# Kernel tuning notes

Hardware: AMD Instinct MI355X
Metric: run time of the kernel (lower is better)

The kernel has to match this reference:

```python
import jax, jax.numpy as jnp
import numpy as np

B, S, H, L, NH, DH, V, FF, WD, W = 16, 512, 768, 12, 12, 64, 30522, 3072, 256, 255
T = S - 1


def layer_norm(x, s, b, eps=1e-12):
    m = jnp.mean(x, -1, keepdims=True)
    v = jnp.mean((x - m) ** 2, -1, keepdims=True)
    return (x - m) * jax.lax.rsqrt(v + eps) * s + b


def setup_inputs() -> dict:
    key = jax.random.key(0)
    ks = jax.random.split(key, 20)
    rng = np.random.RandomState(0)
    # ragged structure: words per sentence and wordpieces per word
    sent_lens = rng.randint(128, W + 1, size=B)
    token_lens = np.zeros((B, W), dtype=np.int32)
    for i in range(B):
        token_lens[i, : sent_lens[i]] = rng.randint(1, 3, size=sent_lens[i])
    bert_len = token_lens.sum(1)  # wordpieces per sentence (no CLS/SEP)
    attention_mask = (np.arange(S)[None, :] < (bert_len + 2)[:, None]).astype(np.int32)
    input_ids = rng.randint(0, V, size=(B, S)).astype(np.int32)
    sd = 0.02
    rn = lambda k, sh: jax.random.normal(k, sh, jnp.float32) * sd
    inp = {
        "input_ids": jnp.asarray(input_ids),
        "attention_mask": jnp.asarray(attention_mask),
        "token_lens": jnp.asarray(token_lens),
        "word_emb": rn(ks[0], (V, H)),
        "pos_emb": rn(ks[1], (S, H)),
        "type_emb": rn(ks[2], (2, H)),
        "emb_ln_s": jnp.ones((H,), jnp.float32),
        "emb_ln_b": jnp.zeros((H,), jnp.float32),
        "Wq": rn(ks[3], (L, H, H)), "bq": jnp.zeros((L, H), jnp.float32),
        "Wk": rn(ks[4], (L, H, H)), "bk": jnp.zeros((L, H), jnp.float32),
        "Wv": rn(ks[5], (L, H, H)), "bv": jnp.zeros((L, H), jnp.float32),
        "Wo": rn(ks[6], (L, H, H)), "bo": jnp.zeros((L, H), jnp.float32),
        "ln1_s": jnp.ones((L, H), jnp.float32), "ln1_b": jnp.zeros((L, H), jnp.float32),
        "W1": rn(ks[7], (L, H, FF)), "b1": jnp.zeros((L, FF), jnp.float32),
        "W2": rn(ks[8], (L, FF, H)), "b2": jnp.zeros((L, H), jnp.float32),
        "ln2_s": jnp.ones((L, H), jnp.float32), "ln2_b": jnp.zeros((L, H), jnp.float32),
        "proj_W": rn(ks[9], (H, WD)), "proj_b": jnp.zeros((WD,), jnp.float32),
    }
    return inp


def reference(input_ids, attention_mask, token_lens, word_emb, pos_emb, type_emb,
              emb_ln_s, emb_ln_b, Wq, bq, Wk, bk, Wv, bv, Wo, bo, ln1_s, ln1_b,
              W1, b1, W2, b2, ln2_s, ln2_b, proj_W, proj_b):
    # --- BERT embeddings ---
    h = word_emb[input_ids] + pos_emb[None, :, :] + type_emb[0][None, None, :]
    h = layer_norm(h, emb_ln_s, emb_ln_b)
    att_bias = (1.0 - attention_mask.astype(jnp.float32))[:, None, None, :] * -10000.0

    def block(h, p):
        wq, bq_, wk, bk_, wv, bv_, wo, bo_, l1s, l1b, w1, b1_, w2, b2_, l2s, l2b = p
        q = (h @ wq + bq_).reshape(B, S, NH, DH)
        k = (h @ wk + bk_).reshape(B, S, NH, DH)
        v = (h @ wv + bv_).reshape(B, S, NH, DH)
        scores = jnp.einsum('bqnd,bknd->bnqk', q, k) / np.float32(np.sqrt(DH)) + att_bias
        a = jax.nn.softmax(scores, axis=-1)
        ctx = jnp.einsum('bnqk,bknd->bqnd', a, v).reshape(B, S, H)
        h = layer_norm(h + ctx @ wo + bo_, l1s, l1b)
        f = jax.nn.gelu(h @ w1 + b1_, approximate=False) @ w2 + b2_
        h = layer_norm(h + f, l2s, l2b)
        return h, None

    h, _ = jax.lax.scan(block, h, (Wq, bq, Wk, bk, Wv, bv, Wo, bo, ln1_s, ln1_b,
                                   W1, b1, W2, b2, ln2_s, ln2_b))
    # drop [CLS], project to word_dims
    hid = h[:, 1:, :] @ proj_W + proj_b  # [B, T, WD]
    # --- ragged segment-mean merge (vectorized form of merge_embedding) ---
    cum = jnp.cumsum(token_lens, axis=1)  # [B, W]
    pos = jnp.arange(T)
    word_id = jnp.sum(pos[None, :, None] >= cum[:, None, :], axis=-1)  # token -> word
    valid = pos[None, :] < cum[:, -1][:, None]  # token within bert_len
    onehot = ((word_id[:, :, None] == jnp.arange(W)[None, None, :]) & valid[:, :, None]).astype(hid.dtype)
    sums = jnp.einsum('btw,btd->bwd', onehot, hid)  # [B, W, WD]
    means = sums / jnp.maximum(token_lens, 1)[:, :, None].astype(hid.dtype)
    word_masks = (token_lens > 0).astype(jnp.float32)  # [B, W]
    return means, word_masks
```

## Files before the change

### kernel.cpp

```cpp
#include <hip/hip_runtime.h>
#include <stdint.h>

#define B_ 16
#define S_ 512
#define H_ 768
#define L_ 12
#define NH_ 12
#define DH_ 64
#define FF_ 3072
#define WD_ 256
#define W_ 255
#define MTOK_ (B_*S_)
#define QKVN_ 2304
#define MPADR_ 128

typedef _Float16 f16;
typedef _Float16 f16x8 __attribute__((ext_vector_type(8)));
typedef _Float16 f16x4 __attribute__((ext_vector_type(4)));
typedef _Float16 f16x2 __attribute__((ext_vector_type(2)));
typedef float f32x4 __attribute__((ext_vector_type(4)));

__device__ __forceinline__ float gelu_fast(float x) {
  float u = x * (1.0f + 0.044715f * x * x);
  float e = __expf(-1.5957691216f * u);
  return __fdividef(x, 1.0f + e);
}

__device__ __forceinline__ void gload16(const f16* g, f16* l) {
  __builtin_amdgcn_global_load_lds(
      (const __attribute__((address_space(1))) void*)g,
      (__attribute__((address_space(3))) void*)l, 16, 0, 0);
}

template<int BM, int BN, int ACT, int OUTF16, int BIAS, int QKVW>
__global__ __launch_bounds__(256) void gemm2_k(
    const f16* __restrict__ A, const f16* __restrict__ Bm, void* __restrict__ Cv,
    const float* __restrict__ bias, f16* __restrict__ vTp,
    const int* __restrict__ rowmap, const int* __restrict__ meta,
    int lda, int ldb, int ldc, int K, float scale)
{
  constexpr int MI = BM / 32;
  constexpr int NI = BN / 32;
  const int gx = gridDim.x;
  int flat = blockIdx.y * gx + blockIdx.x;
  const int nlive = (meta[1] / BM) * gx;
  if (flat >= nlive) return;
  {
    int q = nlive >> 3, r = nlive & 7;
    int xcd = flat & 7, idx = flat >> 3;
    flat = (xcd < r ? xcd * (q + 1) : r * (q + 1) + (xcd - r) * q) + idx;
  }
  const int row0 = (flat / gx) * BM;
  const int col0 = (flat % gx) * BN;

  __shared__ __align__(16) f16 lA[2][BM * 64];
  __shared__ __align__(16) f16 lB[2][BN * 64];
  const int lane = threadIdx.x & 63;
  const int wave = threadIdx.x >> 6;
  const int wr = wave >> 1, wc = wave & 1;
  const int srow = lane >> 3;
  const int scol = lane & 7;
  const int cs = scol ^ srow;

  int arow[BM / 32];
#pragma unroll
  for (int i = 0; i < BM / 32; ++i)
    arow[i] = rowmap[row0 + (wave * (BM / 32) + i) * 8 + srow];

  auto stage = [&](int p, int k0) {
#pragma unroll
    for (int i = 0; i < BM / 32; ++i) {
      int seg = wave * (BM / 32) + i;
      gload16(&A[(size_t)arow[i] * lda + k0 + cs * 8], &lA[p][seg * 512]);
    }
#pragma unroll
    for (int i = 0; i < BN / 32; ++i) {
      int seg = wave * (BN / 32) + i;
      gload16(&Bm[(size_t)(col0 + seg * 8 + srow) * ldb + k0 + cs * 8], &lB[p][seg * 512]);
    }
  };

  f32x4 acc[MI][NI] = {};
  const int nt = K >> 6;
  stage(0, 0);
  const int rl = lane & 15, g = lane >> 4;
  for (int t = 0; t < nt; ++t) {
    __syncthreads();
    if (t + 1 < nt) stage((t + 1) & 1, (t + 1) * 64);
    const int p = t & 1;
#pragma unroll
    for (int c = 0; c < 2; ++c) {
      f16x8 af[MI], bf[NI];
#pragma unroll
      for (int mi = 0; mi < MI; ++mi) {
        int r = wr * (MI * 16) + mi * 16 + rl;
        int u = (c * 4 + g) ^ (r & 7);
        af[mi] = *(const f16x8*)&lA[p][r * 64 + u * 8];
      }
#pragma unroll
      for (int ni = 0; ni < NI; ++ni) {
        int r = wc * (NI * 16) + ni * 16 + rl;
        int u = (c * 4 + g) ^ (r & 7);
        bf[ni] = *(const f16x8*)&lB[p][r * 64 + u * 8];
      }
#pragma unroll
      for (int mi = 0; mi < MI; ++mi)
#pragma unroll
        for (int ni = 0; ni < NI; ++ni)
          acc[mi][ni] = __builtin_amdgcn_mfma_f32_16x16x32_f16(af[mi], bf[ni], acc[mi][ni], 0, 0, 0);
    }
  }
  const int cl = lane & 15;
  const int rq = (lane >> 4) * 4;
#pragma unroll
  for (int mi = 0; mi < MI; ++mi) {
    const int4 rm4 = *(const int4*)&rowmap[row0 + wr * (MI * 16) + mi * 16 + rq];
    const int rows[4] = { rm4.x, rm4.y, rm4.z, rm4.w };
    const bool contig = (rm4.w == rm4.x + 3) && ((rm4.x & 3) == 0);
#pragma unroll
    for (int ni = 0; ni < NI; ++ni) {
      int col = col0 + wc * (NI * 16) + ni * 16 + cl;
      float bv = 0.f;
      if constexpr (BIAS) bv = bias[col];
      if constexpr (QKVW) {
        if (col >= 2 * H_) {
          int vc = col - 2 * H_;
          int h = vc >> 6, d = vc & 63;
          if (contig) {
            if (rm4.x < MTOK_) {
              int b = rm4.x >> 9, s = rm4.x & (S_ - 1);
              f16x4 o4;
#pragma unroll
              for (int r = 0; r < 4; ++r) o4[r] = (f16)(acc[mi][ni][r] * scale + bv);
              *(f16x4*)&vTp[(((size_t)(b * NH_ + h)) * DH_ + d) * S_ + s] = o4;
            }
          } else {
#pragma unroll
            for (int r = 0; r < 4; ++r) {
              int orow = rows[r];
              if (orow < MTOK_) {
                int b = orow >> 9, s = orow & (S_ - 1);
                vTp[(((size_t)(b * NH_ + h)) * DH_ + d) * S_ + s] = (f16)(acc[mi][ni][r] * scale + bv);
              }
            }
          }
          continue;
        }
      }
#pragma unroll
      for (int r = 0; r < 4; ++r) {
        float v = acc[mi][ni][r] * scale + bv;
        if constexpr (ACT == 1) v = gelu_fast(v);
        if constexpr (OUTF16) {
          ((f16*)Cv)[(size_t)rows[r] * ldc + col] = (f16)v;
        } else {
          ((float*)Cv)[(size_t)rows[r] * ldc + col] = v;
        }
      }
    }
  }
}

__global__ __launch_bounds__(256) void fattn_k(
    const f16* __restrict__ qkv, const f16* __restrict__ vT,
    f16* __restrict__ ctx, const int* __restrict__ lenp)
{
  const int bh = blockIdx.x, qt = blockIdx.y;
  const int b = bh / NH_, h = bh - b * NH_;
  const int L = lenp[b];
  if ((qt << 7) >= L) return;
  const int nkt = (L + 63) >> 6;
  const int lane = threadIdx.x & 63, wave = threadIdx.x >> 6;
  const int rl = lane & 15, g = lane >> 4;
  const int srow = lane >> 3, scol = lane & 7;
  const int cs = scol ^ srow;

  __shared__ __align__(16) f16 lK[2][64 * 64];
  __shared__ __align__(16) f16 lV[2][64 * 64];
  __shared__ __align__(16) f16 lP[128 * 72];

  auto stage = [&](int p, int kt) {
#pragma unroll
    for (int i = 0; i < 2; ++i) {
      int seg = wave * 2 + i;
      int r = seg * 8 + srow;
      gload16(&qkv[((size_t)b * S_ + kt * 64 + r) * QKVN_ + H_ + h * DH_ + cs * 8], &lK[p][seg * 512]);
      gload16(&vT[((size_t)bh * DH_ + r) * S_ + kt * 64 + cs * 8], &lV[p][seg * 512]);
    }
  };

  const size_t qrow0 = (size_t)b * S_ + qt * 128 + wave * 32;
  f16x8 qf[2][2];
#pragma unroll
  for (int bq = 0; bq < 2; ++bq)
#pragma unroll
    for (int kc = 0; kc < 2; ++kc)
      qf[bq][kc] = *(const f16x8*)&qkv[(qrow0 + bq * 16 + rl) * QKVN_ + h * DH_ + kc * 32 + g * 8];

  float lsum[2] = {0.f, 0.f};
  f32x4 accO[2][4] = {};

  stage(0, 0);
  for (int kt = 0; kt < nkt; ++kt) {
    __syncthreads();
    if (kt + 1 < nkt) stage((kt + 1) & 1, kt + 1);
    const int p = kt & 1;

    f32x4 accS[4][2] = {};
#pragma unroll
    for (int kc = 0; kc < 2; ++kc) {
#pragma unroll
      for (int ak = 0; ak < 4; ++ak) {
        int row = ak * 16 + rl;
        int u = (kc * 4 + g) ^ (row & 7);
        f16x8 kf = *(const f16x8*)&lK[p][row * 64 + u * 8];
#pragma unroll
        for (int bq = 0; bq < 2; ++bq)
          accS[ak][bq] = __builtin_amdgcn_mfma_f32_16x16x32_f16(kf, qf[bq][kc], accS[ak][bq], 0, 0, 0);
      }
    }

    const int kvb = kt * 64 + g * 4;
#pragma unroll
    for (int bq = 0; bq < 2; ++bq) {
      float pv[16];
      float ps = 0.f;
#pragma unroll
      for (int ak = 0; ak < 4; ++ak)
#pragma unroll
        for (int r = 0; r < 4; ++r) {
          float s = accS[ak][bq][r] * 0.125f;
          float pp = (kvb + ak * 16 + r < L) ? __expf(s) : 0.f;
          pv[ak * 4 + r] = pp;
          ps += pp;
        }
      ps += __shfl_xor(ps, 16);
      ps += __shfl_xor(ps, 32);
      lsum[bq] += ps;
      const int qrow = wave * 32 + bq * 16 + rl;
#pragma unroll
      for (int ak = 0; ak < 4; ++ak)
#pragma unroll
        for (int r2 = 0; r2 < 2; ++r2) {
          f16x2 pk = { (f16)pv[ak * 4 + r2 * 2], (f16)pv[ak * 4 + r2 * 2 + 1] };
          *(f16x2*)&lP[qrow * 72 + ak * 16 + g * 4 + r2 * 2] = pk;
        }
    }
#pragma unroll
    for (int kc = 0; kc < 2; ++kc) {
      f16x8 pa[2], vf[4];
#pragma unroll
      for (int aq = 0; aq < 2; ++aq) {
        int prow = wave * 32 + aq * 16 + rl;
        pa[aq] = *(const f16x8*)&lP[prow * 72 + kc * 32 + g * 8];
      }
#pragma unroll
      for (int bd = 0; bd < 4; ++bd) {
        int vrow = bd * 16 + rl;
        int u = (kc * 4 + g) ^ (vrow & 7);
        vf[bd] = *(const f16x8*)&lV[p][vrow * 64 + u * 8];
      }
#pragma unroll
      for (int aq = 0; aq < 2; ++aq)
#pragma unroll
        for (int bd = 0; bd < 4; ++bd)
          accO[aq][bd] = __builtin_amdgcn_mfma_f32_16x16x32_f16(pa[aq], vf[bd], accO[aq][bd], 0, 0, 0);
    }
  }

  float linv[2] = { 1.f / lsum[0], 1.f / lsum[1] };
  const size_t orow0 = (size_t)b * S_ + qt * 128 + wave * 32;
#pragma unroll
  for (int aq = 0; aq < 2; ++aq)
#pragma unroll
    for (int r = 0; r < 4; ++r) {
      float li = __shfl(linv[aq], (lane & 48) | (g * 4 + r));
      int q = aq * 16 + g * 4 + r;
#pragma unroll
      for (int bd = 0; bd < 4; ++bd)
        ctx[(orow0 + q) * H_ + h * DH_ + bd * 16 + rl] = (f16)(accO[aq][bd][r] * li);
    }
}

template<typename TI>
__global__ __launch_bounds__(256) void transpose_f16_k(
    const TI* __restrict__ in, f16* __restrict__ out,
    int ldin, int ldout, long i1, long o1)
{
  const int z = blockIdx.z;
  in  += (size_t)z * i1;
  out += (size_t)z * o1;
  __shared__ float t[32][33];
  const int kt = blockIdx.y * 32, nt = blockIdx.x * 32;
  const int tx = threadIdx.x & 31, tg = threadIdx.x >> 5;
#pragma unroll
  for (int i = 0; i < 4; ++i) {
    int k = tg * 4 + i;
    t[k][tx] = (float)in[(size_t)(kt + k) * ldin + nt + tx];
  }
  __syncthreads();
#pragma unroll
  for (int i = 0; i < 4; ++i) {
    int n = tg * 4 + i;
    out[(size_t)(nt + n) * ldout + kt + tx] = (f16)t[tx][n];
  }
}

__global__ void bias_cat_k(const float* __restrict__ bq, const float* __restrict__ bk,
                           const float* __restrict__ bv, float* __restrict__ out) {
  const int l = blockIdx.y;
  const int j = blockIdx.x * 256 + threadIdx.x;
  float v = (j < H_) ? bq[l * H_ + j] : (j < 2 * H_) ? bk[l * H_ + j - H_] : bv[l * H_ + j - 2 * H_];
  out[l * QKVN_ + j] = v;
}

__global__ __launch_bounds__(256) void embed_ln_k(
    const int* __restrict__ ids, const float* __restrict__ wemb,
    const float* __restrict__ pemb, const float* __restrict__ temb,
    const float* __restrict__ lns, const float* __restrict__ lnb,
    float* __restrict__ h32, f16* __restrict__ h16)
{
  const int row = blockIdx.x * 4 + (threadIdx.x >> 6);
  const int lane = threadIdx.x & 63;
  const int s = row & (S_ - 1);
  const float4* wp = (const float4*)(wemb + (size_t)ids[row] * H_);
  const float4* pp = (const float4*)(pemb + (size_t)s * H_);
  const float4* tp = (const float4*)temb;
  float4 x[3]; float sm = 0.f, sq = 0.f;
#pragma unroll
  for (int j = 0; j < 3; ++j) {
    int i4 = lane + 64 * j;
    float4 a = wp[i4], bb = pp[i4], c = tp[i4];
    float4 v; v.x = a.x + bb.x + c.x; v.y = a.y + bb.y + c.y;
    v.z = a.z + bb.z + c.z; v.w = a.w + bb.w + c.w;
    x[j] = v;
    sm += v.x + v.y + v.z + v.w;
    sq += v.x * v.x + v.y * v.y + v.z * v.z + v.w * v.w;
  }
#pragma unroll
  for (int o = 32; o > 0; o >>= 1) { sm += __shfl_xor(sm, o); sq += __shfl_xor(sq, o); }
  float mean = sm * (1.f / H_);
  float inv = rsqrtf(sq * (1.f / H_) - mean * mean + 1e-12f);
  float4* hw = (float4*)(h32 + (size_t)row * H_);
  f16* ho = h16 + (size_t)row * H_;
#pragma unroll
  for (int j = 0; j < 3; ++j) {
    int i4 = lane + 64 * j;
    float4 sc = ((const float4*)lns)[i4], bi = ((const float4*)lnb)[i4];
    float4 v = x[j], y;
    y.x = (v.x - mean) * inv * sc.x + bi.x;
    y.y = (v.y - mean) * inv * sc.y + bi.y;
    y.z = (v.z - mean) * inv * sc.z + bi.z;
    y.w = (v.w - mean) * inv * sc.w + bi.w;
    hw[i4] = y;
    f16x4 o4 = {(f16)y.x, (f16)y.y, (f16)y.z, (f16)y.w};
    *(f16x4*)&ho[i4 * 4] = o4;
  }
}

__global__ __launch_bounds__(256) void ln_res_k(
    float* __restrict__ h32, const f16* __restrict__ tmp,
    const float* __restrict__ lns, const float* __restrict__ lnb,
    f16* __restrict__ h16, const int* __restrict__ rowmap, const int* __restrict__ meta)
{
  const int crow = blockIdx.x * 4 + (threadIdx.x >> 6);
  if (crow >= meta[0]) return;
  const int row = rowmap[crow];
  const int lane = threadIdx.x & 63;
  const float4* hp = (const float4*)(h32 + (size_t)row * H_);
  const f16x4* tp = (const f16x4*)(tmp + (size_t)row * H_);
  float4 x[3]; float sm = 0.f, sq = 0.f;
#pragma unroll
  for (int j = 0; j < 3; ++j) {
    int i4 = lane + 64 * j;
    float4 a = hp[i4];
    f16x4 tv = tp[i4];
    float4 v; v.x = a.x + (float)tv[0]; v.y = a.y + (float)tv[1];
    v.z = a.z + (float)tv[2]; v.w = a.w + (float)tv[3];
    x[j] = v;
    sm += v.x + v.y + v.z + v.w;
    sq += v.x * v.x + v.y * v.y + v.z * v.z + v.w * v.w;
  }
#pragma unroll
  for (int o = 32; o > 0; o >>= 1) { sm += __shfl_xor(sm, o); sq += __shfl_xor(sq, o); }
  float mean = sm * (1.f / H_);
  float inv = rsqrtf(sq * (1.f / H_) - mean * mean + 1e-12f);
  float4* hw = (float4*)(h32 + (size_t)row * H_);
  f16* ho = h16 + (size_t)row * H_;
#pragma unroll
  for (int j = 0; j < 3; ++j) {
    int i4 = lane + 64 * j;
    float4 sc = ((const float4*)lns)[i4], bi = ((const float4*)lnb)[i4];
    float4 v = x[j], y;
    y.x = (v.x - mean) * inv * sc.x + bi.x;
    y.y = (v.y - mean) * inv * sc.y + bi.y;
    y.z = (v.z - mean) * inv * sc.z + bi.z;
    y.w = (v.w - mean) * inv * sc.w + bi.w;
    hw[i4] = y;
    f16x4 o4 = {(f16)y.x, (f16)y.y, (f16)y.z, (f16)y.w};
    *(f16x4*)&ho[i4 * 4] = o4;
  }
}

__global__ void len_k(const int* __restrict__ mask, int* __restrict__ len) {
  const int b = blockIdx.x;
  const int t = threadIdx.x;
  __shared__ int red[512];
  red[t] = mask[b * S_ + t]; __syncthreads();
  for (int o = 256; o > 0; o >>= 1) { if (t < o) red[t] += red[t + o]; __syncthreads(); }
  if (t == 0) len[b] = red[0];
}

__global__ void rowmap_k(const int* __restrict__ len, int* __restrict__ meta,
                         int* __restrict__ rowmap) {
  __shared__ int cum[17];
  if (threadIdx.x == 0) {
    int c = 0; cum[0] = 0;
    for (int b = 0; b < B_; ++b) { c += len[b]; cum[b + 1] = c; }
    meta[0] = c;
    meta[1] = (c + 127) & ~127;
  }
  __syncthreads();
  const int Mv = cum[16];
  for (int i = threadIdx.x; i < MTOK_ + MPADR_; i += 256) {
    int orig;
    if (i < Mv) {
      int b = 0;
#pragma unroll
      for (int t = 1; t <= 16; ++t) b += (i >= cum[t]) ? 1 : 0;
      orig = b * S_ + (i - cum[b]);
    } else {
      int d = i - Mv;
      orig = MTOK_ + (d < MPADR_ ? d : MPADR_ - 1);
    }
    rowmap[i] = orig;
  }
}

__global__ __launch_bounds__(256) void merge_k(
    const float* __restrict__ proj, const int* __restrict__ tl,
    float* __restrict__ means, float* __restrict__ masks)
{
  const int w = blockIdx.x, b = blockIdx.y;
  const int t = threadIdx.x;
  __shared__ int red[256];
  int part = 0;
  for (int j = t; j < w; j += 256) part += tl[b * W_ + j];
  red[t] = part; __syncthreads();
  for (int o = 128; o > 0; o >>= 1) { if (t < o) red[t] += red[t + o]; __syncthreads(); }
  const int start = red[0];
  const int len = tl[b * W_ + w];
  float s = 0.f;
  for (int l = 0; l < len; ++l)
    s += proj[((size_t)b * S_ + 1 + start + l) * WD_ + t];
  means[((size_t)b * W_ + w) * WD_ + t] = (len > 0) ? s / (float)len : 0.f;
  if (t == 0) masks[b * W_ + w] = (len > 0) ? 1.f : 0.f;
}

extern "C" void kernel_launch(void* const* d_in, const int* in_sizes, int n_in,
                              void* d_out, int out_size, void* d_ws, size_t ws_size,
                              hipStream_t stream)
{
  (void)in_sizes; (void)n_in; (void)out_size;
  const int*   ids   = (const int*)d_in[0];
  const int*   amask = (const int*)d_in[1];
  const int*   tlens = (const int*)d_in[2];
  const float* wemb  = (const float*)d_in[3];
  const float* pemb  = (const float*)d_in[4];
  const float* temb  = (const float*)d_in[5];
  const float* elns  = (const float*)d_in[6];
  const float* elnb  = (const float*)d_in[7];
  const float* Wq = (const float*)d_in[8];  const float* bq = (const float*)d_in[9];
  const float* Wk = (const float*)d_in[10]; const float* bk = (const float*)d_in[11];
  const float* Wv = (const float*)d_in[12]; const float* bv = (const float*)d_in[13];
  const float* Wo = (const float*)d_in[14]; const float* bo = (const float*)d_in[15];
  const float* l1s = (const float*)d_in[16]; const float* l1b = (const float*)d_in[17];
  const float* W1 = (const float*)d_in[18]; const float* b1 = (const float*)d_in[19];
  const float* W2 = (const float*)d_in[20]; const float* b2 = (const float*)d_in[21];
  const float* l2s = (const float*)d_in[22]; const float* l2b = (const float*)d_in[23];
  const float* pW = (const float*)d_in[24]; const float* pb = (const float*)d_in[25];

  const int MR = MTOK_ + MPADR_;
  char* ws = (char*)d_ws;
  size_t off = 0;
  auto alloc = [&](size_t n) { void* r = ws + off; off += (n + 255) & ~(size_t)255; return r; };
  float* h32   = (float*)alloc((size_t)MR * H_ * 4);
  f16*   h16   = (f16*)alloc((size_t)MR * H_ * 2);
  f16*   qkv   = (f16*)alloc((size_t)MR * QKVN_ * 2);
  f16*   ctx16 = (f16*)alloc((size_t)MR * H_ * 2);
  f16*   vT    = (f16*)alloc((size_t)B_ * NH_ * DH_ * S_ * 2);
  f16*   ff16  = (f16*)alloc((size_t)MR * FF_ * 2);
  f16*   tmp16 = (f16*)alloc((size_t)MR * H_ * 2);
  float* proj32 = (float*)alloc((size_t)MR * WD_ * 4);
  f16*   pwT   = (f16*)alloc((size_t)WD_ * H_ * 2);
  float* bqkv  = (float*)alloc((size_t)L_ * QKVN_ * 4);
  int*   lenb  = (int*)alloc(256);
  int*   meta  = (int*)alloc(256);
  int*   rowmap = (int*)alloc((size_t)MR * 4);

  const size_t wqkv_sz = (size_t)QKVN_ * H_ * 2;
  const size_t wo_sz   = (size_t)H_ * H_ * 2;
  const size_t w1_sz   = (size_t)H_ * FF_ * 2;
  const size_t w2_sz   = (size_t)FF_ * H_ * 2;
  const size_t per_layer_w = wqkv_sz + wo_sz + w1_sz + w2_sz;
  const bool big = ws_size >= off + (size_t)L_ * per_layer_w + 8192;
  const int nz = big ? L_ : 1;
  f16* wqkv0 = (f16*)alloc((size_t)nz * wqkv_sz);
  f16* wo0   = (f16*)alloc((size_t)nz * wo_sz);
  f16* w10   = (f16*)alloc((size_t)nz * w1_sz);
  f16* w20   = (f16*)alloc((size_t)nz * w2_sz);

  len_k<<<B_, 512, 0, stream>>>(amask, lenb);
  rowmap_k<<<1, 256, 0, stream>>>(lenb, meta, rowmap);
  embed_ln_k<<<MTOK_ / 4, 256, 0, stream>>>(ids, wemb, pemb, temb, elns, elnb, h32, h16);
  transpose_f16_k<float><<<dim3(WD_/32, H_/32, 1), 256, 0, stream>>>(pW, pwT, WD_, H_, 0, 0);
  bias_cat_k<<<dim3(QKVN_/256, L_), 256, 0, stream>>>(bq, bk, bv, bqkv);

  if (big) {
    transpose_f16_k<float><<<dim3(H_/32, H_/32, L_), 256, 0, stream>>>(
        Wq, wqkv0,                   H_, H_, (long)H_*H_, (long)QKVN_*H_);
    transpose_f16_k<float><<<dim3(H_/32, H_/32, L_), 256, 0, stream>>>(
        Wk, wqkv0 + (size_t)H_*H_,   H_, H_, (long)H_*H_, (long)QKVN_*H_);
    transpose_f16_k<float><<<dim3(H_/32, H_/32, L_), 256, 0, stream>>>(
        Wv, wqkv0 + (size_t)2*H_*H_, H_, H_, (long)H_*H_, (long)QKVN_*H_);
    transpose_f16_k<float><<<dim3(H_/32, H_/32, L_), 256, 0, stream>>>(
        Wo, wo0, H_, H_, (long)H_*H_, (long)H_*H_);
    transpose_f16_k<float><<<dim3(FF_/32, H_/32, L_), 256, 0, stream>>>(
        W1, w10, FF_, H_, (long)H_*FF_, (long)H_*FF_);
    transpose_f16_k<float><<<dim3(H_/32, FF_/32, L_), 256, 0, stream>>>(
        W2, w20, H_, FF_, (long)FF_*H_, (long)FF_*H_);
  }

  for (int l = 0; l < L_; ++l) {
    f16* wqkv_l = wqkv0 + (size_t)(big ? l : 0) * QKVN_ * H_;
    f16* wo_l   = wo0   + (size_t)(big ? l : 0) * H_ * H_;
    f16* w1_l   = w10   + (size_t)(big ? l : 0) * H_ * FF_;
    f16* w2_l   = w20   + (size_t)(big ? l : 0) * FF_ * H_;
    if (!big) {
      transpose_f16_k<float><<<dim3(H_/32, H_/32, 1), 256, 0, stream>>>(
          Wq + (size_t)l*H_*H_, wqkv_l,                   H_, H_, 0, 0);
      transpose_f16_k<float><<<dim3(H_/32, H_/32, 1), 256, 0, stream>>>(
          Wk + (size_t)l*H_*H_, wqkv_l + (size_t)H_*H_,   H_, H_, 0, 0);
      transpose_f16_k<float><<<dim3(H_/32, H_/32, 1), 256, 0, stream>>>(
          Wv + (size_t)l*H_*H_, wqkv_l + (size_t)2*H_*H_, H_, H_, 0, 0);
      transpose_f16_k<float><<<dim3(H_/32, H_/32, 1), 256, 0, stream>>>(
          Wo + (size_t)l*H_*H_, wo_l, H_, H_, 0, 0);
      transpose_f16_k<float><<<dim3(FF_/32, H_/32, 1), 256, 0, stream>>>(
          W1 + (size_t)l*H_*FF_, w1_l, FF_, H_, 0, 0);
      transpose_f16_k<float><<<dim3(H_/32, FF_/32, 1), 256, 0, stream>>>(
          W2 + (size_t)l*FF_*H_, w2_l, H_, FF_, 0, 0);
    }
    gemm2_k<64,128,0,1,1,1><<<dim3(QKVN_/128, MTOK_/64, 1), 256, 0, stream>>>(
        h16, wqkv_l, qkv, bqkv + (size_t)l*QKVN_, vT, rowmap, meta, H_, H_, QKVN_, H_, 1.0f);
    fattn_k<<<dim3(B_*NH_, S_/128), 256, 0, stream>>>(qkv, vT, ctx16, lenb);
    gemm2_k<64,64,0,1,1,0><<<dim3(H_/64, MTOK_/64, 1), 256, 0, stream>>>(
        ctx16, wo_l, tmp16, bo + (size_t)l*H_, nullptr, rowmap, meta, H_, H_, H_, H_, 1.0f);
    ln_res_k<<<MTOK_/4, 256, 0, stream>>>(h32, tmp16, l1s + (size_t)l*H_, l1b + (size_t)l*H_, h16, rowmap, meta);
    gemm2_k<64,128,1,1,1,0><<<dim3(FF_/128, MTOK_/64, 1), 256, 0, stream>>>(
        h16, w1_l, ff16, b1 + (size_t)l*FF_, nullptr, rowmap, meta, H_, H_, FF_, H_, 1.0f);
    gemm2_k<64,64,0,1,1,0><<<dim3(H_/64, MTOK_/64, 1), 256, 0, stream>>>(
        ff16, w2_l, tmp16, b2 + (size_t)l*H_, nullptr, rowmap, meta, FF_, FF_, H_, FF_, 1.0f);
    ln_res_k<<<MTOK_/4, 256, 0, stream>>>(h32, tmp16, l2s + (size_t)l*H_, l2b + (size_t)l*H_, h16, rowmap, meta);
  }

  gemm2_k<64,64,0,0,1,0><<<dim3(WD_/64, MTOK_/64, 1), 256, 0, stream>>>(
      h16, pwT, proj32, pb, nullptr, rowmap, meta, H_, H_, WD_, H_, 1.0f);
  merge_k<<<dim3(W_, B_), 256, 0, stream>>>(proj32, tlens,
      (float*)d_out, (float*)d_out + (size_t)B_ * W_ * WD_);
}
```

Baseline: 2.410 ms.

## Prefetch two stages ahead with explicit waitcnt/barriers and MFMA priority

The GEMM mainloop now issues loads for tile t+2 after the compute of tile t, and waits with vmcnt counts instead of a full __syncthreads, so more global-to-LDS transfers are in flight while MFMAs run. The attention kernel replaces __syncthreads with a partial vmcnt wait plus an explicit trailing barrier that protects buffer reuse. Both kernels raise wave priority around MFMA blocks with s_setprio and fence the scheduler around the barriers. This relies on hand-counted outstanding-load numbers (LPW, 4), and a wrong count would cause races, while the extra barriers add some sync overhead.

```diff
diff --git a/kernel.cpp b/kernel.cpp
--- a/kernel.cpp
+++ b/kernel.cpp
@@ -20,6 +20,8 @@
 typedef _Float16 f16x2 __attribute__((ext_vector_type(2)));
 typedef float f32x4 __attribute__((ext_vector_type(4)));
 
+#define SCHED_FENCE() __builtin_amdgcn_sched_barrier(0)
+
 __device__ __forceinline__ float gelu_fast(float x) {
   float u = x * (1.0f + 0.044715f * x * x);
   float e = __expf(-1.5957691216f * u);
@@ -41,6 +43,7 @@
 {
   constexpr int MI = BM / 32;
   constexpr int NI = BN / 32;
+  constexpr int LPW = BM / 32 + BN / 32;
   const int gx = gridDim.x;
   int flat = blockIdx.y * gx + blockIdx.x;
   const int nlive = (meta[1] / BM) * gx;
@@ -82,12 +85,17 @@
 
   f32x4 acc[MI][NI] = {};
   const int nt = K >> 6;
+  const int rl = lane & 15, g = lane >> 4;
   stage(0, 0);
-  const int rl = lane & 15, g = lane >> 4;
+  if (nt > 1) stage(1, 64);
   for (int t = 0; t < nt; ++t) {
-    __syncthreads();
-    if (t + 1 < nt) stage((t + 1) & 1, (t + 1) * 64);
+    if (t < nt - 1) { asm volatile("s_waitcnt vmcnt(%0) lgkmcnt(0)" :: "i"(LPW) : "memory"); }
+    else            { asm volatile("s_waitcnt vmcnt(0) lgkmcnt(0)" ::: "memory"); }
+    SCHED_FENCE();
+    __builtin_amdgcn_s_barrier();
+    SCHED_FENCE();
     const int p = t & 1;
+    __builtin_amdgcn_s_setprio(1);
 #pragma unroll
     for (int c = 0; c < 2; ++c) {
       f16x8 af[MI], bf[NI];
@@ -109,6 +117,13 @@
         for (int ni = 0; ni < NI; ++ni)
           acc[mi][ni] = __builtin_amdgcn_mfma_f32_16x16x32_f16(af[mi], bf[ni], acc[mi][ni], 0, 0, 0);
     }
+    __builtin_amdgcn_s_setprio(0);
+    SCHED_FENCE();
+    asm volatile("s_waitcnt lgkmcnt(0)" ::: "memory");
+    SCHED_FENCE();
+    __builtin_amdgcn_s_barrier();
+    SCHED_FENCE();
+    if (t + 2 < nt) stage(p, (t + 2) * 64);
   }
   const int cl = lane & 15;
   const int rq = (lane >> 4) * 4;
@@ -202,11 +217,19 @@
 
   stage(0, 0);
   for (int kt = 0; kt < nkt; ++kt) {
-    __syncthreads();
-    if (kt + 1 < nkt) stage((kt + 1) & 1, kt + 1);
+    if (kt + 1 < nkt) {
+      stage((kt + 1) & 1, kt + 1);
+      asm volatile("s_waitcnt vmcnt(4) lgkmcnt(0)" ::: "memory");
+    } else {
+      asm volatile("s_waitcnt vmcnt(0) lgkmcnt(0)" ::: "memory");
+    }
+    SCHED_FENCE();
+    __builtin_amdgcn_s_barrier();
+    SCHED_FENCE();
     const int p = kt & 1;
 
     f32x4 accS[4][2] = {};
+    __builtin_amdgcn_s_setprio(1);
 #pragma unroll
     for (int kc = 0; kc < 2; ++kc) {
 #pragma unroll
@@ -219,6 +242,7 @@
           accS[ak][bq] = __builtin_amdgcn_mfma_f32_16x16x32_f16(kf, qf[bq][kc], accS[ak][bq], 0, 0, 0);
       }
     }
+    __builtin_amdgcn_s_setprio(0);
 
     const int kvb = kt * 64 + g * 4;
 #pragma unroll
@@ -246,6 +270,7 @@
           *(f16x2*)&lP[qrow * 72 + ak * 16 + g * 4 + r2 * 2] = pk;
         }
     }
+    __builtin_amdgcn_s_setprio(1);
 #pragma unroll
     for (int kc = 0; kc < 2; ++kc) {
       f16x8 pa[2], vf[4];
@@ -266,6 +291,12 @@
         for (int bd = 0; bd < 4; ++bd)
           accO[aq][bd] = __builtin_amdgcn_mfma_f32_16x16x32_f16(pa[aq], vf[bd], accO[aq][bd], 0, 0, 0);
     }
+    __builtin_amdgcn_s_setprio(0);
+    SCHED_FENCE();
+    asm volatile("s_waitcnt lgkmcnt(0)" ::: "memory");
+    SCHED_FENCE();
+    __builtin_amdgcn_s_barrier();
+    SCHED_FENCE();
   }
 
   float linv[2] = { 1.f / lsum[0], 1.f / lsum[1] };
```

After: 2.369 ms. No clear change (-1.7%).
